# Optimization experiments

Hardware: AMD Instinct MI355X
Metric: run time of the kernel (lower is better)

The kernel has to match this reference:

```python
import jax, jax.numpy as jnp
import numpy as np

B, N, D, S, H, ITERS = 128, 4096, 64, 7, 128, 3
EPS = 1e-8
LN_EPS = 1e-5


def _ln(x, g, b):
    mu = jnp.mean(x, axis=-1, keepdims=True)
    var = jnp.mean(jnp.square(x - mu), axis=-1, keepdims=True)
    return (x - mu) * jax.lax.rsqrt(var + LN_EPS) * g + b


def setup_inputs() -> dict:
    key = jax.random.key(0)
    ks = jax.random.split(key, 20)
    xav = lambda k, shp: jax.random.normal(k, shp, jnp.float32) * (2.0 / sum(shp[-2:])) ** 0.5
    inp = {
        "inputs": jax.random.normal(ks[0], (B, N, D), jnp.float32),
        "noise_bg": jax.random.normal(ks[1], (B, 1, D), jnp.float32),
        "noise_fg": jax.random.normal(ks[2], (B, S - 1, D), jnp.float32),
        "ln_in_g": jnp.ones((D,), jnp.float32), "ln_in_b": jnp.zeros((D,), jnp.float32),
        "ln_slot_g": jnp.ones((D,), jnp.float32), "ln_slot_b": jnp.zeros((D,), jnp.float32),
        "ln_mlp_g": jnp.ones((D,), jnp.float32), "ln_mlp_b": jnp.zeros((D,), jnp.float32),
        "Wq": xav(ks[3], (D, D)), "Wk": xav(ks[4], (D, D)), "Wv": xav(ks[5], (D, D)),
        "W_ih": xav(ks[6], (3 * D, D)), "W_hh": xav(ks[7], (3 * D, D)),
        "b_ih": jnp.zeros((3 * D,), jnp.float32), "b_hh": jnp.zeros((3 * D,), jnp.float32),
        "mlp_w1": xav(ks[8], (H, D)), "mlp_b1": jnp.zeros((H,), jnp.float32),
        "mlp_w2": xav(ks[9], (D, H)), "mlp_b2": jnp.zeros((D,), jnp.float32),
        "slots_bg_mu": xav(ks[10], (1, 1, D)),
        "slots_bg_log_sigma": xav(ks[11], (1, 1, D)),
        "slots_mu": xav(ks[12], (1, 1, D)),
        "slots_log_sigma": xav(ks[13], (1, 1, D)),
    }
    return inp


def _gru(x, h, W_ih, W_hh, b_ih, b_hh):
    # x, h: [M, D]; PyTorch GRUCell math, gate order r, z, n
    gi = x @ W_ih.T + b_ih
    gh = h @ W_hh.T + b_hh
    i_r, i_z, i_n = jnp.split(gi, 3, axis=-1)
    h_r, h_z, h_n = jnp.split(gh, 3, axis=-1)
    r = jax.nn.sigmoid(i_r + h_r)
    z = jax.nn.sigmoid(i_z + h_z)
    n = jnp.tanh(i_n + r * h_n)
    return (1.0 - z) * n + z * h


def reference(inputs, noise_bg, noise_fg, ln_in_g, ln_in_b, ln_slot_g, ln_slot_b,
              ln_mlp_g, ln_mlp_b, Wq, Wk, Wv, W_ih, W_hh, b_ih, b_hh,
              mlp_w1, mlp_b1, mlp_w2, mlp_b2,
              slots_bg_mu, slots_bg_log_sigma, slots_mu, slots_log_sigma):
    x = _ln(inputs, ln_in_g, ln_in_b)          # [B, N, D]
    k = jnp.einsum('bnd,ed->bne', x, Wk)       # [B, N, D]
    v = jnp.einsum('bnd,ed->bne', x, Wv)

    bg = slots_bg_mu + jnp.exp(slots_bg_log_sigma) * noise_bg   # [B, 1, D]
    fg = slots_mu + jnp.exp(slots_log_sigma) * noise_fg          # [B, S-1, D]
    slots = jnp.concatenate([bg, fg], axis=1)                    # [B, S, D]

    scale = D ** (-0.5)
    for _ in range(ITERS):
        slots_prev = slots
        s = _ln(slots, ln_slot_g, ln_slot_b)
        q = jnp.einsum('bsd,ed->bse', s, Wq)                     # [B, S, D]
        logits = scale * jnp.einsum('bnd,bsd->bns', k, q)        # [B, N, S]
        attn = jax.nn.softmax(logits, axis=-1) + EPS             # softmax over slots
        attn = attn / jnp.sum(attn, axis=1, keepdims=True)       # renorm over inputs
        updates = jnp.einsum('bns,bnd->bsd', attn, v)            # [B, S, D]
        h = _gru(updates.reshape(B * S, D), slots_prev.reshape(B * S, D),
                 W_ih, W_hh, b_ih, b_hh).reshape(B, S, D)
        m = _ln(h, ln_mlp_g, ln_mlp_b)
        m = jax.nn.relu(m @ mlp_w1.T + mlp_b1) @ mlp_w2.T + mlp_b2
        slots = h + m
    return slots
```

## Files before the change

kernel.cpp:

```cpp
#include <hip/hip_runtime.h>

#define BB 128
#define NN 4096
#define DD 64
#define SS 7
#define HH 128
#define N_ITERS 3
#define EPS_ATTN 1e-8f
#define LN_EPS 1e-5f

typedef unsigned short ushortT;
using short8  = __attribute__((ext_vector_type(8))) short;
using floatx4 = __attribute__((ext_vector_type(4))) float;

__device__ __forceinline__ float bf2f(int u) {
    return __builtin_bit_cast(float, (unsigned)(u & 0xffff) << 16);
}
__device__ __forceinline__ ushortT f2bf(float f) {
    unsigned x = __builtin_bit_cast(unsigned, f);
    x = x + 0x7fff + ((x >> 16) & 1);
    return (ushortT)(x >> 16);
}
__device__ __forceinline__ void wave_stats64(float x, float& mu, float& var) {
    float s1 = x, s2 = x * x;
#pragma unroll
    for (int off = 32; off > 0; off >>= 1) {
        s1 += __shfl_xor(s1, off);
        s2 += __shfl_xor(s2, off);
    }
    mu  = s1 * (1.f / 64.f);
    var = s2 * (1.f / 64.f) - mu * mu;
}

__global__ void prep_w(const float* __restrict__ Wk, const float* __restrict__ Wv,
                       const float* __restrict__ Wih, const float* __restrict__ Whh,
                       const float* __restrict__ w1, const float* __restrict__ w2,
                       ushortT* __restrict__ Wkvf, float* __restrict__ WihT,
                       float* __restrict__ WhhT, float* __restrict__ w1T,
                       float* __restrict__ w2T) {
    int i = blockIdx.x * 256 + threadIdx.x;
    if (i < 8192) {
        int c2 = i >> 9, lane = (i >> 3) & 63, j = i & 7;
        int tile = c2 >> 1, cc = c2 & 1;
        int qd = lane >> 4, m = lane & 15;
        int row = tile * 16 + m;
        int col = cc * 32 + qd * 8 + j;
        float v = (row < 64) ? Wk[row * 64 + col] : Wv[(row - 64) * 64 + col];
        Wkvf[i] = f2bf(v);
    } else if (i < 20480) {
        int j = i - 8192; int e = j >> 6, d = j & 63;
        WihT[d * 192 + e] = Wih[j];
    } else if (i < 32768) {
        int j = i - 20480; int e = j >> 6, d = j & 63;
        WhhT[d * 192 + e] = Whh[j];
    } else if (i < 40960) {
        int j = i - 32768; int e = j >> 6, d = j & 63;
        w1T[d * 128 + e] = w1[j];
    } else if (i < 49152) {
        int j = i - 40960; int e = j >> 7, h = j & 127;
        w2T[h * 64 + e] = w2[j];
    }
}

__global__ __launch_bounds__(256) void kv_proj(const float* __restrict__ x,
                                               const float* __restrict__ g,
                                               const float* __restrict__ bta,
                                               const ushortT* __restrict__ Wkvf,
                                               ushortT* __restrict__ kg,
                                               ushortT* __restrict__ vtg) {
    int t = threadIdx.x, w = t >> 6, lane = t & 63;
    long row0 = (long)blockIdx.x << 6;
    int sub = t & 3, r = t >> 2;
    __shared__ ushortT lds_a[64][72];

    const float* xr = x + (row0 + r) * 64 + sub * 16;
    float4 xa[4];
#pragma unroll
    for (int c = 0; c < 4; ++c) xa[c] = *reinterpret_cast<const float4*>(xr + c * 4);
    float s1 = 0.f, s2 = 0.f;
#pragma unroll
    for (int c = 0; c < 4; ++c) {
        s1 += xa[c].x + xa[c].y + xa[c].z + xa[c].w;
        s2 += xa[c].x * xa[c].x + xa[c].y * xa[c].y +
              xa[c].z * xa[c].z + xa[c].w * xa[c].w;
    }
    s1 += __shfl_xor(s1, 1); s2 += __shfl_xor(s2, 1);
    s1 += __shfl_xor(s1, 2); s2 += __shfl_xor(s2, 2);
    float mu = s1 * (1.f / 64.f);
    float var = s2 * (1.f / 64.f) - mu * mu;
    float rs = rsqrtf(var + LN_EPS);
    unsigned un[8];
#pragma unroll
    for (int c = 0; c < 4; ++c) {
        float4 g4 = *reinterpret_cast<const float4*>(g + sub * 16 + c * 4);
        float4 b4 = *reinterpret_cast<const float4*>(bta + sub * 16 + c * 4);
        float n0 = (xa[c].x - mu) * rs * g4.x + b4.x;
        float n1 = (xa[c].y - mu) * rs * g4.y + b4.y;
        float n2 = (xa[c].z - mu) * rs * g4.z + b4.z;
        float n3 = (xa[c].w - mu) * rs * g4.w + b4.w;
        un[c * 2]     = (unsigned)f2bf(n0) | ((unsigned)f2bf(n1) << 16);
        un[c * 2 + 1] = (unsigned)f2bf(n2) | ((unsigned)f2bf(n3) << 16);
    }
    *reinterpret_cast<uint4*>(&lds_a[r][sub * 16]) =
        make_uint4(un[0], un[1], un[2], un[3]);
    *reinterpret_cast<uint4*>(&lds_a[r][sub * 16 + 8]) =
        make_uint4(un[4], un[5], un[6], un[7]);

    int m = lane & 15, qd = lane >> 4;
    short8 bk[4][2];
#pragma unroll
    for (int tt = 0; tt < 4; ++tt)
#pragma unroll
        for (int c = 0; c < 2; ++c)
            bk[tt][c] = *reinterpret_cast<const short8*>(
                Wkvf + (tt * 2 + c) * 512 + lane * 8);
    __syncthreads();

    short8 af[2];
#pragma unroll
    for (int c = 0; c < 2; ++c)
        af[c] = *reinterpret_cast<const short8*>(&lds_a[w * 16 + m][c * 32 + qd * 8]);

    floatx4 ak[4];
#pragma unroll
    for (int tt = 0; tt < 4; ++tt) ak[tt] = (floatx4){0.f, 0.f, 0.f, 0.f};
#pragma unroll
    for (int tt = 0; tt < 4; ++tt)
#pragma unroll
        for (int c = 0; c < 2; ++c)
            ak[tt] = __builtin_amdgcn_mfma_f32_16x16x32_bf16(bk[tt][c], af[c],
                                                             ak[tt], 0, 0, 0);
    long kbase = ((long)blockIdx.x << 12) + w * 1024 + lane * 4;
#pragma unroll
    for (int tt = 0; tt < 4; ++tt) {
        uint2 u;
        u.x = (unsigned)f2bf(ak[tt][0]) | ((unsigned)f2bf(ak[tt][1]) << 16);
        u.y = (unsigned)f2bf(ak[tt][2]) | ((unsigned)f2bf(ak[tt][3]) << 16);
        *reinterpret_cast<uint2*>(kg + kbase + tt * 256) = u;
    }

    short8 bv[4][2];
#pragma unroll
    for (int tt = 0; tt < 4; ++tt)
#pragma unroll
        for (int c = 0; c < 2; ++c)
            bv[tt][c] = *reinterpret_cast<const short8*>(
                Wkvf + ((tt + 4) * 2 + c) * 512 + lane * 8);
    floatx4 av[4];
#pragma unroll
    for (int tt = 0; tt < 4; ++tt) av[tt] = (floatx4){0.f, 0.f, 0.f, 0.f};
#pragma unroll
    for (int tt = 0; tt < 4; ++tt)
#pragma unroll
        for (int c = 0; c < 2; ++c)
            av[tt] = __builtin_amdgcn_mfma_f32_16x16x32_bf16(af[c], bv[tt][c],
                                                             av[tt], 0, 0, 0);
    int ks  = (((int)(row0 & 127)) + w * 16) >> 5;
    int qd2 = (w * 2 + (qd >> 1)) & 3;
    long vbase = (((long)blockIdx.x >> 1) << 13) + ks * 512 + qd2 * 128 + m * 8 +
                 (qd & 1) * 4;
#pragma unroll
    for (int tt = 0; tt < 4; ++tt) {
        uint2 u;
        u.x = (unsigned)f2bf(av[tt][0]) | ((unsigned)f2bf(av[tt][1]) << 16);
        u.y = (unsigned)f2bf(av[tt][2]) | ((unsigned)f2bf(av[tt][3]) << 16);
        *reinterpret_cast<uint2*>(vtg + vbase + tt * 2048) = u;
    }
}

__global__ __launch_bounds__(256) void attn_kernel(const ushortT* __restrict__ kg,
                                                   const ushortT* __restrict__ vtg,
                                                   const float* __restrict__ qbuf,
                                                   float* __restrict__ num_p,
                                                   float* __restrict__ den_p) {
    int t = threadIdx.x;
    int ck = blockIdx.x;
    int b = ck >> 5;
    __shared__ float   q_lds[7][68];
    __shared__ ushortT p_lds[16][136];
    __shared__ float   den_w[4][8];
    int w = t >> 6, lane = t & 63, m = lane & 15, qd = lane >> 4;
    int sub = t & 3, rr = t >> 2;

    uint2 kf[2][4];
#pragma unroll
    for (int p = 0; p < 2; ++p) {
        const ushortT* kp = kg + ((long)(ck * 2 + p) << 12) + w * 1024 +
                            sub * 256 + (lane >> 2) * 4;
#pragma unroll
        for (int dq = 0; dq < 4; ++dq)
            kf[p][dq] = *reinterpret_cast<const uint2*>(kp + dq * 64);
    }
    const ushortT* vb = vtg + ((long)ck << 13) + w * 2048 + lane * 8;
    short8 bf[4];
#pragma unroll
    for (int ks = 0; ks < 4; ++ks)
        bf[ks] = *reinterpret_cast<const short8*>(vb + ks * 512);
    for (int i = t; i < 448; i += 256) q_lds[i >> 6][i & 63] = qbuf[b * 448 + i];
    __syncthreads();

    float dreg0 = 0.f, dreg1 = 0.f;
    int s0 = sub * 2;
#pragma unroll
    for (int p = 0; p < 2; ++p) {
        int row = p * 64 + rr;
        float kx[16];
#pragma unroll
        for (int dq = 0; dq < 4; ++dq) {
            kx[dq * 4 + 0] = bf2f(kf[p][dq].x);
            kx[dq * 4 + 1] = bf2f(kf[p][dq].x >> 16);
            kx[dq * 4 + 2] = bf2f(kf[p][dq].y);
            kx[dq * 4 + 3] = bf2f(kf[p][dq].y >> 16);
        }
        float lg[7];
#pragma unroll
        for (int s = 0; s < 7; ++s) {
            const float4* qp = reinterpret_cast<const float4*>(&q_lds[s][sub << 4]);
            float acc = 0.f;
#pragma unroll
            for (int c = 0; c < 4; ++c) {
                float4 qv = qp[c];
                acc += kx[c * 4 + 0] * qv.x + kx[c * 4 + 1] * qv.y +
                       kx[c * 4 + 2] * qv.z + kx[c * 4 + 3] * qv.w;
            }
            lg[s] = acc;
        }
#pragma unroll
        for (int s = 0; s < 7; ++s) {
            lg[s] += __shfl_xor(lg[s], 1);
            lg[s] += __shfl_xor(lg[s], 2);
        }
        float mx = lg[0];
#pragma unroll
        for (int s = 1; s < 7; ++s) mx = fmaxf(mx, lg[s]);
        float sum = 0.f, ps[7];
#pragma unroll
        for (int s = 0; s < 7; ++s) { ps[s] = __expf(lg[s] - mx); sum += ps[s]; }
        float inv = 1.f / sum;
        float p0 = 0.f, p1 = 0.f;
#pragma unroll
        for (int s = 0; s < 7; ++s) {
            float pv = ps[s] * inv + EPS_ATTN;
            if (s == s0)     p0 = pv;
            if (s == s0 + 1) p1 = pv;
        }
        ushortT pb0 = f2bf(p0);
        p_lds[s0][row] = pb0;
        dreg0 += bf2f(pb0);
        if (sub < 3) {
            ushortT pb1 = f2bf(p1);
            p_lds[s0 + 1][row] = pb1;
            dreg1 += bf2f(pb1);
        }
    }
#pragma unroll
    for (int off = 4; off < 64; off <<= 1) {
        dreg0 += __shfl_xor(dreg0, off);
        dreg1 += __shfl_xor(dreg1, off);
    }
    if (lane < 4) {
        den_w[w][2 * lane] = dreg0;
        if (lane < 3) den_w[w][2 * lane + 1] = dreg1;
    }
    __syncthreads();

    floatx4 acc = (floatx4){0.f, 0.f, 0.f, 0.f};
#pragma unroll
    for (int ks = 0; ks < 4; ++ks) {
        short8 af = *reinterpret_cast<const short8*>(&p_lds[m][ks * 32 + qd * 8]);
        acc = __builtin_amdgcn_mfma_f32_16x16x32_bf16(af, bf[ks], acc, 0, 0, 0);
    }
#pragma unroll
    for (int r = 0; r < 4; ++r) {
        int s = qd * 4 + r;
        if (s < 7) num_p[((long)ck * 7 + s) * 64 + w * 16 + m] = acc[r];
    }
    if (t < 7) den_p[ck * 8 + t] = den_w[0][t] + den_w[1][t] + den_w[2][t] + den_w[3][t];
}

__global__ __launch_bounds__(448) void slot_update_q(
    int mode,
    const float* __restrict__ num_p, const float* __restrict__ den_p,
    float* __restrict__ slots,
    const float* __restrict__ nbg, const float* __restrict__ nfg,
    const float* __restrict__ bgmu, const float* __restrict__ bgls,
    const float* __restrict__ fmu, const float* __restrict__ fls,
    const float* __restrict__ WihT, const float* __restrict__ WhhT,
    const float* __restrict__ bih, const float* __restrict__ bhh,
    const float* __restrict__ lng, const float* __restrict__ lnb,
    const float* __restrict__ w1T, const float* __restrict__ b1,
    const float* __restrict__ w2T, const float* __restrict__ b2,
    const float* __restrict__ Wq,
    const float* __restrict__ sg, const float* __restrict__ sb,
    float* __restrict__ qbuf, float* __restrict__ outp) {
    int b = blockIdx.x, t = threadIdx.x, s = t >> 6, l = t & 63;
    __shared__ float WqT[64 * 65];
    __shared__ float updL[7][64], hprevL[7][64], mnL[7][64], m1L[7][128], xnL[7][64];
    if (mode != 2)
        for (int i = t; i < 4096; i += 448)
            WqT[(i & 63) * 65 + (i >> 6)] = Wq[i];
    float res;
    if (mode == 0) {
        float v;
        if (s == 0) v = bgmu[l] + __expf(bgls[l]) * nbg[b * 64 + l];
        else        v = fmu[l]  + __expf(fls[l])  * nfg[(b * 6 + s - 1) * 64 + l];
        res = v;
        __syncthreads();
    } else {
        float nsum = 0.f, dsum = 0.f;
#pragma unroll 4
        for (int c = 0; c < 32; ++c) {
            nsum += num_p[((long)(b * 32 + c) * 7 + s) * 64 + l];
            dsum += den_p[(b * 32 + c) * 8 + s];
        }
        float hp = slots[(b * 7 + s) * 64 + l];
        updL[s][l]   = nsum / dsum;
        hprevL[s][l] = hp;
        __syncthreads();
        float gi0 = bih[l], gi1 = bih[64 + l], gi2 = bih[128 + l];
        float gh0 = bhh[l], gh1 = bhh[64 + l], gh2 = bhh[128 + l];
#pragma unroll 8
        for (int d = 0; d < 64; ++d) {
            float u = updL[s][d], hh = hprevL[s][d];
            gi0 += u * WihT[d * 192 + l];
            gi1 += u * WihT[d * 192 + 64 + l];
            gi2 += u * WihT[d * 192 + 128 + l];
            gh0 += hh * WhhT[d * 192 + l];
            gh1 += hh * WhhT[d * 192 + 64 + l];
            gh2 += hh * WhhT[d * 192 + 128 + l];
        }
        float r = 1.f / (1.f + __expf(-(gi0 + gh0)));
        float z = 1.f / (1.f + __expf(-(gi1 + gh1)));
        float n = tanhf(gi2 + r * gh2);
        float h = (1.f - z) * n + z * hp;
        float mu, var;
        wave_stats64(h, mu, var);
        mnL[s][l] = (h - mu) * rsqrtf(var + LN_EPS) * lng[l] + lnb[l];
        float a0 = b1[l], a1 = b1[64 + l];
#pragma unroll 8
        for (int d = 0; d < 64; ++d) {
            float mv = mnL[s][d];
            a0 += mv * w1T[d * 128 + l];
            a1 += mv * w1T[d * 128 + 64 + l];
        }
        m1L[s][l]      = fmaxf(a0, 0.f);
        m1L[s][64 + l] = fmaxf(a1, 0.f);
        float a2 = b2[l];
#pragma unroll 8
        for (int h2 = 0; h2 < 128; ++h2) a2 += m1L[s][h2] * w2T[h2 * 64 + l];
        res = h + a2;
    }
    slots[(b * 7 + s) * 64 + l] = res;
    if (mode == 2) {
        outp[(b * 7 + s) * 64 + l] = res;
        return;
    }
    float mu, var;
    wave_stats64(res, mu, var);
    xnL[s][l] = (res - mu) * rsqrtf(var + LN_EPS) * sg[l] + sb[l];
    float acc = 0.f;
#pragma unroll 8
    for (int d = 0; d < 64; ++d) acc += xnL[s][d] * WqT[d * 65 + l];
    qbuf[(b * 7 + s) * 64 + l] = acc * 0.125f;
}

extern "C" void kernel_launch(void* const* d_in, const int* in_sizes, int n_in,
                              void* d_out, int out_size, void* d_ws, size_t ws_size,
                              hipStream_t stream) {
    const float* inputs    = (const float*)d_in[0];
    const float* noise_bg  = (const float*)d_in[1];
    const float* noise_fg  = (const float*)d_in[2];
    const float* ln_in_g   = (const float*)d_in[3];
    const float* ln_in_b   = (const float*)d_in[4];
    const float* ln_slot_g = (const float*)d_in[5];
    const float* ln_slot_b = (const float*)d_in[6];
    const float* ln_mlp_g  = (const float*)d_in[7];
    const float* ln_mlp_b  = (const float*)d_in[8];
    const float* Wq        = (const float*)d_in[9];
    const float* Wk        = (const float*)d_in[10];
    const float* Wv        = (const float*)d_in[11];
    const float* W_ih      = (const float*)d_in[12];
    const float* W_hh      = (const float*)d_in[13];
    const float* b_ih      = (const float*)d_in[14];
    const float* b_hh      = (const float*)d_in[15];
    const float* mlp_w1    = (const float*)d_in[16];
    const float* mlp_b1    = (const float*)d_in[17];
    const float* mlp_w2    = (const float*)d_in[18];
    const float* mlp_b2    = (const float*)d_in[19];
    const float* sbg_mu    = (const float*)d_in[20];
    const float* sbg_ls    = (const float*)d_in[21];
    const float* s_mu      = (const float*)d_in[22];
    const float* s_ls      = (const float*)d_in[23];

    char* ws = (char*)d_ws;
    size_t off = 0;
    auto alloc = [&](size_t bytes) {
        void* p = ws + off;
        off += (bytes + 255) & ~(size_t)255;
        return p;
    };
    ushortT* kg    = (ushortT*)alloc((size_t)BB * NN * 64 * 2);
    ushortT* vtg   = (ushortT*)alloc((size_t)BB * NN * 64 * 2);
    ushortT* Wkvf  = (ushortT*)alloc(8192 * 2);
    float* slots   = (float*)alloc(57344 * 4);
    float* qbuf    = (float*)alloc(57344 * 4);
    float* num_p   = (float*)alloc((size_t)4096 * 7 * 64 * 4);
    float* den_p   = (float*)alloc(4096 * 8 * 4);
    float* WihT    = (float*)alloc(12288 * 4);
    float* WhhT    = (float*)alloc(12288 * 4);
    float* w1T     = (float*)alloc(8192 * 4);
    float* w2T     = (float*)alloc(8192 * 4);
    if (off > ws_size) return;

    prep_w<<<192, 256, 0, stream>>>(Wk, Wv, W_ih, W_hh, mlp_w1, mlp_w2,
                                    Wkvf, WihT, WhhT, w1T, w2T);
    slot_update_q<<<128, 448, 0, stream>>>(0, num_p, den_p, slots,
                                           noise_bg, noise_fg, sbg_mu, sbg_ls,
                                           s_mu, s_ls, WihT, WhhT, b_ih, b_hh,
                                           ln_mlp_g, ln_mlp_b, w1T, mlp_b1,
                                           w2T, mlp_b2, Wq, ln_slot_g, ln_slot_b,
                                           qbuf, (float*)d_out);
    kv_proj<<<8192, 256, 0, stream>>>(inputs, ln_in_g, ln_in_b, Wkvf, kg, vtg);
    for (int it = 0; it < N_ITERS; ++it) {
        attn_kernel<<<4096, 256, 0, stream>>>(kg, vtg, qbuf, num_p, den_p);
        slot_update_q<<<128, 448, 0, stream>>>((it == N_ITERS - 1) ? 2 : 1,
                                               num_p, den_p, slots,
                                               noise_bg, noise_fg, sbg_mu, sbg_ls,
                                               s_mu, s_ls, WihT, WhhT, b_ih, b_hh,
                                               ln_mlp_g, ln_mlp_b, w1T, mlp_b1,
                                               w2T, mlp_b2, Wq, ln_slot_g, ln_slot_b,
                                               qbuf, (float*)d_out);
    }
}
```

Baseline: 399.4 us.

## Fold Wk and Wv projections into slot-side math, attend directly on normalized inputs

Removes the separate K/V projection kernel. The logits are computed as xn·(Wkᵀq), with q pre-multiplied by Wk in the slot kernel, and the attention-weighted sum is taken over xn and then multiplied by Wv once per slot. The first attention pass fuses the input layernorm and stores a bf16 normalized copy of the inputs, which later passes reuse. This replaces two bf16 K/V tensors with one, so each iteration reads half the data. The cost is an LDS transpose of xn inside each attention block and small extra matvecs in the slot update.

```diff
diff --git a/kernel.cpp b/kernel.cpp
--- a/kernel.cpp
+++ b/kernel.cpp
@@ -13,8 +13,8 @@
 using short8  = __attribute__((ext_vector_type(8))) short;
 using floatx4 = __attribute__((ext_vector_type(4))) float;
 
-__device__ __forceinline__ float bf2f(int u) {
-    return __builtin_bit_cast(float, (unsigned)(u & 0xffff) << 16);
+__device__ __forceinline__ float bf2f(unsigned u) {
+    return __builtin_bit_cast(float, (u & 0xffffu) << 16);
 }
 __device__ __forceinline__ ushortT f2bf(float f) {
     unsigned x = __builtin_bit_cast(unsigned, f);
@@ -32,190 +32,123 @@
     var = s2 * (1.f / 64.f) - mu * mu;
 }
 
-__global__ void prep_w(const float* __restrict__ Wk, const float* __restrict__ Wv,
-                       const float* __restrict__ Wih, const float* __restrict__ Whh,
+__global__ void prep_w(const float* __restrict__ Wih, const float* __restrict__ Whh,
                        const float* __restrict__ w1, const float* __restrict__ w2,
-                       ushortT* __restrict__ Wkvf, float* __restrict__ WihT,
-                       float* __restrict__ WhhT, float* __restrict__ w1T,
-                       float* __restrict__ w2T) {
+                       const float* __restrict__ Wv,
+                       float* __restrict__ WihT, float* __restrict__ WhhT,
+                       float* __restrict__ w1T, float* __restrict__ w2T,
+                       float* __restrict__ WvT) {
     int i = blockIdx.x * 256 + threadIdx.x;
-    if (i < 8192) {
-        int c2 = i >> 9, lane = (i >> 3) & 63, j = i & 7;
-        int tile = c2 >> 1, cc = c2 & 1;
-        int qd = lane >> 4, m = lane & 15;
-        int row = tile * 16 + m;
-        int col = cc * 32 + qd * 8 + j;
-        float v = (row < 64) ? Wk[row * 64 + col] : Wv[(row - 64) * 64 + col];
-        Wkvf[i] = f2bf(v);
-    } else if (i < 20480) {
-        int j = i - 8192; int e = j >> 6, d = j & 63;
-        WihT[d * 192 + e] = Wih[j];
+    if (i < 12288) {
+        int e = i >> 6, d = i & 63;
+        WihT[d * 192 + e] = Wih[i];
+    } else if (i < 24576) {
+        int j = i - 12288; int e = j >> 6, d = j & 63;
+        WhhT[d * 192 + e] = Whh[j];
     } else if (i < 32768) {
-        int j = i - 20480; int e = j >> 6, d = j & 63;
-        WhhT[d * 192 + e] = Whh[j];
+        int j = i - 24576; int e = j >> 6, d = j & 63;
+        w1T[d * 128 + e] = w1[j];
     } else if (i < 40960) {
-        int j = i - 32768; int e = j >> 6, d = j & 63;
-        w1T[d * 128 + e] = w1[j];
-    } else if (i < 49152) {
-        int j = i - 40960; int e = j >> 7, h = j & 127;
+        int j = i - 32768; int e = j >> 7, h = j & 127;
         w2T[h * 64 + e] = w2[j];
-    }
-}
-
-__global__ __launch_bounds__(256) void kv_proj(const float* __restrict__ x,
-                                               const float* __restrict__ g,
-                                               const float* __restrict__ bta,
-                                               const ushortT* __restrict__ Wkvf,
-                                               ushortT* __restrict__ kg,
-                                               ushortT* __restrict__ vtg) {
-    int t = threadIdx.x, w = t >> 6, lane = t & 63;
-    long row0 = (long)blockIdx.x << 6;
-    int sub = t & 3, r = t >> 2;
-    __shared__ ushortT lds_a[64][72];
-
-    const float* xr = x + (row0 + r) * 64 + sub * 16;
-    float4 xa[4];
-#pragma unroll
-    for (int c = 0; c < 4; ++c) xa[c] = *reinterpret_cast<const float4*>(xr + c * 4);
-    float s1 = 0.f, s2 = 0.f;
-#pragma unroll
-    for (int c = 0; c < 4; ++c) {
-        s1 += xa[c].x + xa[c].y + xa[c].z + xa[c].w;
-        s2 += xa[c].x * xa[c].x + xa[c].y * xa[c].y +
-              xa[c].z * xa[c].z + xa[c].w * xa[c].w;
-    }
-    s1 += __shfl_xor(s1, 1); s2 += __shfl_xor(s2, 1);
-    s1 += __shfl_xor(s1, 2); s2 += __shfl_xor(s2, 2);
-    float mu = s1 * (1.f / 64.f);
-    float var = s2 * (1.f / 64.f) - mu * mu;
-    float rs = rsqrtf(var + LN_EPS);
-    unsigned un[8];
-#pragma unroll
-    for (int c = 0; c < 4; ++c) {
-        float4 g4 = *reinterpret_cast<const float4*>(g + sub * 16 + c * 4);
-        float4 b4 = *reinterpret_cast<const float4*>(bta + sub * 16 + c * 4);
-        float n0 = (xa[c].x - mu) * rs * g4.x + b4.x;
-        float n1 = (xa[c].y - mu) * rs * g4.y + b4.y;
-        float n2 = (xa[c].z - mu) * rs * g4.z + b4.z;
-        float n3 = (xa[c].w - mu) * rs * g4.w + b4.w;
-        un[c * 2]     = (unsigned)f2bf(n0) | ((unsigned)f2bf(n1) << 16);
-        un[c * 2 + 1] = (unsigned)f2bf(n2) | ((unsigned)f2bf(n3) << 16);
-    }
-    *reinterpret_cast<uint4*>(&lds_a[r][sub * 16]) =
-        make_uint4(un[0], un[1], un[2], un[3]);
-    *reinterpret_cast<uint4*>(&lds_a[r][sub * 16 + 8]) =
-        make_uint4(un[4], un[5], un[6], un[7]);
-
-    int m = lane & 15, qd = lane >> 4;
-    short8 bk[4][2];
-#pragma unroll
-    for (int tt = 0; tt < 4; ++tt)
-#pragma unroll
-        for (int c = 0; c < 2; ++c)
-            bk[tt][c] = *reinterpret_cast<const short8*>(
-                Wkvf + (tt * 2 + c) * 512 + lane * 8);
-    __syncthreads();
-
-    short8 af[2];
-#pragma unroll
-    for (int c = 0; c < 2; ++c)
-        af[c] = *reinterpret_cast<const short8*>(&lds_a[w * 16 + m][c * 32 + qd * 8]);
-
-    floatx4 ak[4];
-#pragma unroll
-    for (int tt = 0; tt < 4; ++tt) ak[tt] = (floatx4){0.f, 0.f, 0.f, 0.f};
-#pragma unroll
-    for (int tt = 0; tt < 4; ++tt)
-#pragma unroll
-        for (int c = 0; c < 2; ++c)
-            ak[tt] = __builtin_amdgcn_mfma_f32_16x16x32_bf16(bk[tt][c], af[c],
-                                                             ak[tt], 0, 0, 0);
-    long kbase = ((long)blockIdx.x << 12) + w * 1024 + lane * 4;
-#pragma unroll
-    for (int tt = 0; tt < 4; ++tt) {
-        uint2 u;
-        u.x = (unsigned)f2bf(ak[tt][0]) | ((unsigned)f2bf(ak[tt][1]) << 16);
-        u.y = (unsigned)f2bf(ak[tt][2]) | ((unsigned)f2bf(ak[tt][3]) << 16);
-        *reinterpret_cast<uint2*>(kg + kbase + tt * 256) = u;
-    }
-
-    short8 bv[4][2];
-#pragma unroll
-    for (int tt = 0; tt < 4; ++tt)
-#pragma unroll
-        for (int c = 0; c < 2; ++c)
-            bv[tt][c] = *reinterpret_cast<const short8*>(
-                Wkvf + ((tt + 4) * 2 + c) * 512 + lane * 8);
-    floatx4 av[4];
-#pragma unroll
-    for (int tt = 0; tt < 4; ++tt) av[tt] = (floatx4){0.f, 0.f, 0.f, 0.f};
-#pragma unroll
-    for (int tt = 0; tt < 4; ++tt)
-#pragma unroll
-        for (int c = 0; c < 2; ++c)
-            av[tt] = __builtin_amdgcn_mfma_f32_16x16x32_bf16(af[c], bv[tt][c],
-                                                             av[tt], 0, 0, 0);
-    int ks  = (((int)(row0 & 127)) + w * 16) >> 5;
-    int qd2 = (w * 2 + (qd >> 1)) & 3;
-    long vbase = (((long)blockIdx.x >> 1) << 13) + ks * 512 + qd2 * 128 + m * 8 +
-                 (qd & 1) * 4;
-#pragma unroll
-    for (int tt = 0; tt < 4; ++tt) {
-        uint2 u;
-        u.x = (unsigned)f2bf(av[tt][0]) | ((unsigned)f2bf(av[tt][1]) << 16);
-        u.y = (unsigned)f2bf(av[tt][2]) | ((unsigned)f2bf(av[tt][3]) << 16);
-        *reinterpret_cast<uint2*>(vtg + vbase + tt * 2048) = u;
-    }
-}
-
-__global__ __launch_bounds__(256) void attn_kernel(const ushortT* __restrict__ kg,
-                                                   const ushortT* __restrict__ vtg,
-                                                   const float* __restrict__ qbuf,
-                                                   float* __restrict__ num_p,
-                                                   float* __restrict__ den_p) {
+    } else if (i < 45056) {
+        int j = i - 40960; int d = j >> 6, e = j & 63;
+        WvT[e * 64 + d] = Wv[j];
+    }
+}
+
+__global__ __launch_bounds__(256) void attn_kernel(
+    int first,
+    const float* __restrict__ x,
+    const float* __restrict__ lng, const float* __restrict__ lnb,
+    ushortT* __restrict__ xnf,
+    const float* __restrict__ qkbuf,
+    float* __restrict__ pxn_p, float* __restrict__ den_p) {
     int t = threadIdx.x;
-    int ck = blockIdx.x;
-    int b = ck >> 5;
-    __shared__ float   q_lds[7][68];
+    int ck = blockIdx.x, b = ck >> 5;
+    int w = t >> 6, lane = t & 63, m = lane & 15, qd = lane >> 4;
+    int sub = t & 3, rr = t >> 2;
+    __shared__ float   qk_lds[7][68];
+    __shared__ ushortT xnT[64][136];
     __shared__ ushortT p_lds[16][136];
     __shared__ float   den_w[4][8];
-    int w = t >> 6, lane = t & 63, m = lane & 15, qd = lane >> 4;
-    int sub = t & 3, rr = t >> 2;
-
-    uint2 kf[2][4];
-#pragma unroll
-    for (int p = 0; p < 2; ++p) {
-        const ushortT* kp = kg + ((long)(ck * 2 + p) << 12) + w * 1024 +
-                            sub * 256 + (lane >> 2) * 4;
-#pragma unroll
-        for (int dq = 0; dq < 4; ++dq)
-            kf[p][dq] = *reinterpret_cast<const uint2*>(kp + dq * 64);
-    }
-    const ushortT* vb = vtg + ((long)ck << 13) + w * 2048 + lane * 8;
-    short8 bf[4];
-#pragma unroll
-    for (int ks = 0; ks < 4; ++ks)
-        bf[ks] = *reinterpret_cast<const short8*>(vb + ks * 512);
-    for (int i = t; i < 448; i += 256) q_lds[i >> 6][i & 63] = qbuf[b * 448 + i];
+
+    unsigned xw[2][8];
+    if (first) {
+        float4 g4[4], b4[4];
+#pragma unroll
+        for (int c = 0; c < 4; ++c) {
+            g4[c] = *reinterpret_cast<const float4*>(lng + sub * 16 + c * 4);
+            b4[c] = *reinterpret_cast<const float4*>(lnb + sub * 16 + c * 4);
+        }
+#pragma unroll
+        for (int pass = 0; pass < 2; ++pass) {
+            const float* xr = x + ((long)ck * 128 + pass * 64 + rr) * 64 + sub * 16;
+            float4 xa[4];
+#pragma unroll
+            for (int c = 0; c < 4; ++c)
+                xa[c] = *reinterpret_cast<const float4*>(xr + c * 4);
+            float s1 = 0.f, s2 = 0.f;
+#pragma unroll
+            for (int c = 0; c < 4; ++c) {
+                s1 += xa[c].x + xa[c].y + xa[c].z + xa[c].w;
+                s2 += xa[c].x * xa[c].x + xa[c].y * xa[c].y +
+                      xa[c].z * xa[c].z + xa[c].w * xa[c].w;
+            }
+            s1 += __shfl_xor(s1, 1); s2 += __shfl_xor(s2, 1);
+            s1 += __shfl_xor(s1, 2); s2 += __shfl_xor(s2, 2);
+            float mu = s1 * (1.f / 64.f);
+            float var = s2 * (1.f / 64.f) - mu * mu;
+            float rs = rsqrtf(var + LN_EPS);
+#pragma unroll
+            for (int c = 0; c < 4; ++c) {
+                float n0 = (xa[c].x - mu) * rs * g4[c].x + b4[c].x;
+                float n1 = (xa[c].y - mu) * rs * g4[c].y + b4[c].y;
+                float n2 = (xa[c].z - mu) * rs * g4[c].z + b4[c].z;
+                float n3 = (xa[c].w - mu) * rs * g4[c].w + b4[c].w;
+                xw[pass][c * 2]     = (unsigned)f2bf(n0) | ((unsigned)f2bf(n1) << 16);
+                xw[pass][c * 2 + 1] = (unsigned)f2bf(n2) | ((unsigned)f2bf(n3) << 16);
+            }
+            ushortT* xp = xnf + (long)ck * 8192 + pass * 4096 + t * 16;
+            *reinterpret_cast<uint4*>(xp) =
+                make_uint4(xw[pass][0], xw[pass][1], xw[pass][2], xw[pass][3]);
+            *reinterpret_cast<uint4*>(xp + 8) =
+                make_uint4(xw[pass][4], xw[pass][5], xw[pass][6], xw[pass][7]);
+        }
+    } else {
+#pragma unroll
+        for (int pass = 0; pass < 2; ++pass) {
+            const ushortT* xp = xnf + (long)ck * 8192 + pass * 4096 + t * 16;
+            uint4 u0 = *reinterpret_cast<const uint4*>(xp);
+            uint4 u1 = *reinterpret_cast<const uint4*>(xp + 8);
+            xw[pass][0] = u0.x; xw[pass][1] = u0.y;
+            xw[pass][2] = u0.z; xw[pass][3] = u0.w;
+            xw[pass][4] = u1.x; xw[pass][5] = u1.y;
+            xw[pass][6] = u1.z; xw[pass][7] = u1.w;
+        }
+    }
+    for (int i = t; i < 448; i += 256) qk_lds[i >> 6][i & 63] = qkbuf[b * 448 + i];
     __syncthreads();
 
     float dreg0 = 0.f, dreg1 = 0.f;
     int s0 = sub * 2;
 #pragma unroll
-    for (int p = 0; p < 2; ++p) {
-        int row = p * 64 + rr;
+    for (int pass = 0; pass < 2; ++pass) {
+        int row = pass * 64 + rr;
+#pragma unroll
+        for (int j = 0; j < 16; ++j)
+            xnT[sub * 16 + j][row] =
+                (ushortT)(xw[pass][j >> 1] >> ((j & 1) * 16));
         float kx[16];
 #pragma unroll
-        for (int dq = 0; dq < 4; ++dq) {
-            kx[dq * 4 + 0] = bf2f(kf[p][dq].x);
-            kx[dq * 4 + 1] = bf2f(kf[p][dq].x >> 16);
-            kx[dq * 4 + 2] = bf2f(kf[p][dq].y);
-            kx[dq * 4 + 3] = bf2f(kf[p][dq].y >> 16);
+        for (int j = 0; j < 8; ++j) {
+            kx[2 * j]     = bf2f(xw[pass][j]);
+            kx[2 * j + 1] = bf2f(xw[pass][j] >> 16);
         }
         float lg[7];
 #pragma unroll
         for (int s = 0; s < 7; ++s) {
-            const float4* qp = reinterpret_cast<const float4*>(&q_lds[s][sub << 4]);
+            const float4* qp = reinterpret_cast<const float4*>(&qk_lds[s][sub << 4]);
             float acc = 0.f;
 #pragma unroll
             for (int c = 0; c < 4; ++c) {
@@ -268,19 +201,20 @@
 #pragma unroll
     for (int ks = 0; ks < 4; ++ks) {
         short8 af = *reinterpret_cast<const short8*>(&p_lds[m][ks * 32 + qd * 8]);
-        acc = __builtin_amdgcn_mfma_f32_16x16x32_bf16(af, bf[ks], acc, 0, 0, 0);
+        short8 bf = *reinterpret_cast<const short8*>(&xnT[w * 16 + m][ks * 32 + qd * 8]);
+        acc = __builtin_amdgcn_mfma_f32_16x16x32_bf16(af, bf, acc, 0, 0, 0);
     }
 #pragma unroll
     for (int r = 0; r < 4; ++r) {
         int s = qd * 4 + r;
-        if (s < 7) num_p[((long)ck * 7 + s) * 64 + w * 16 + m] = acc[r];
+        if (s < 7) pxn_p[((long)ck * 7 + s) * 64 + w * 16 + m] = acc[r];
     }
     if (t < 7) den_p[ck * 8 + t] = den_w[0][t] + den_w[1][t] + den_w[2][t] + den_w[3][t];
 }
 
 __global__ __launch_bounds__(448) void slot_update_q(
     int mode,
-    const float* __restrict__ num_p, const float* __restrict__ den_p,
+    const float* __restrict__ pxn_p, const float* __restrict__ den_p,
     float* __restrict__ slots,
     const float* __restrict__ nbg, const float* __restrict__ nfg,
     const float* __restrict__ bgmu, const float* __restrict__ bgls,
@@ -290,12 +224,14 @@
     const float* __restrict__ lng, const float* __restrict__ lnb,
     const float* __restrict__ w1T, const float* __restrict__ b1,
     const float* __restrict__ w2T, const float* __restrict__ b2,
+    const float* __restrict__ WvT, const float* __restrict__ Wk,
     const float* __restrict__ Wq,
     const float* __restrict__ sg, const float* __restrict__ sb,
-    float* __restrict__ qbuf, float* __restrict__ outp) {
+    float* __restrict__ qkbuf, float* __restrict__ outp) {
     int b = blockIdx.x, t = threadIdx.x, s = t >> 6, l = t & 63;
     __shared__ float WqT[64 * 65];
-    __shared__ float updL[7][64], hprevL[7][64], mnL[7][64], m1L[7][128], xnL[7][64];
+    __shared__ float pxnL[7][64], updL[7][64], hprevL[7][64], mnL[7][64],
+                     xnL[7][64], qL[7][64], m1L[7][128];
     if (mode != 2)
         for (int i = t; i < 4096; i += 448)
             WqT[(i & 63) * 65 + (i >> 6)] = Wq[i];
@@ -307,15 +243,19 @@
         res = v;
         __syncthreads();
     } else {
-        float nsum = 0.f, dsum = 0.f;
+        float psum = 0.f, dsum = 0.f;
 #pragma unroll 4
         for (int c = 0; c < 32; ++c) {
-            nsum += num_p[((long)(b * 32 + c) * 7 + s) * 64 + l];
+            psum += pxn_p[((long)(b * 32 + c) * 7 + s) * 64 + l];
             dsum += den_p[(b * 32 + c) * 8 + s];
         }
+        pxnL[s][l] = psum;
         float hp = slots[(b * 7 + s) * 64 + l];
-        updL[s][l]   = nsum / dsum;
         hprevL[s][l] = hp;
+        float nm = 0.f;
+#pragma unroll 8
+        for (int e = 0; e < 64; ++e) nm += pxnL[s][e] * WvT[e * 64 + l];
+        updL[s][l] = nm / dsum;
         __syncthreads();
         float gi0 = bih[l], gi1 = bih[64 + l], gi2 = bih[128 + l];
         float gh0 = bhh[l], gh1 = bhh[64 + l], gh2 = bhh[128 + l];
@@ -358,10 +298,14 @@
     float mu, var;
     wave_stats64(res, mu, var);
     xnL[s][l] = (res - mu) * rsqrtf(var + LN_EPS) * sg[l] + sb[l];
-    float acc = 0.f;
-#pragma unroll 8
-    for (int d = 0; d < 64; ++d) acc += xnL[s][d] * WqT[d * 65 + l];
-    qbuf[(b * 7 + s) * 64 + l] = acc * 0.125f;
+    float qv = 0.f;
+#pragma unroll 8
+    for (int d = 0; d < 64; ++d) qv += xnL[s][d] * WqT[d * 65 + l];
+    qL[s][l] = qv * 0.125f;
+    float qk = 0.f;
+#pragma unroll 8
+    for (int e = 0; e < 64; ++e) qk += qL[s][e] * Wk[e * 64 + l];
+    qkbuf[(b * 7 + s) * 64 + l] = qk;
 }
 
 extern "C" void kernel_launch(void* const* d_in, const int* in_sizes, int n_in,
@@ -399,36 +343,38 @@
         off += (bytes + 255) & ~(size_t)255;
         return p;
     };
-    ushortT* kg    = (ushortT*)alloc((size_t)BB * NN * 64 * 2);
-    ushortT* vtg   = (ushortT*)alloc((size_t)BB * NN * 64 * 2);
-    ushortT* Wkvf  = (ushortT*)alloc(8192 * 2);
+    ushortT* xnf   = (ushortT*)alloc((size_t)BB * NN * 64 * 2);
     float* slots   = (float*)alloc(57344 * 4);
-    float* qbuf    = (float*)alloc(57344 * 4);
-    float* num_p   = (float*)alloc((size_t)4096 * 7 * 64 * 4);
+    float* qkbuf   = (float*)alloc(57344 * 4);
+    float* pxn_p   = (float*)alloc((size_t)4096 * 7 * 64 * 4);
     float* den_p   = (float*)alloc(4096 * 8 * 4);
     float* WihT    = (float*)alloc(12288 * 4);
     float* WhhT    = (float*)alloc(12288 * 4);
     float* w1T     = (float*)alloc(8192 * 4);
     float* w2T     = (float*)alloc(8192 * 4);
+    float* WvT     = (float*)alloc(4096 * 4);
     if (off > ws_size) return;
 
-    prep_w<<<192, 256, 0, stream>>>(Wk, Wv, W_ih, W_hh, mlp_w1, mlp_w2,
-                                    Wkvf, WihT, WhhT, w1T, w2T);
-    slot_update_q<<<128, 448, 0, stream>>>(0, num_p, den_p, slots,
+    prep_w<<<176, 256, 0, stream>>>(W_ih, W_hh, mlp_w1, mlp_w2, Wv,
+                                    WihT, WhhT, w1T, w2T, WvT);
+    slot_update_q<<<128, 448, 0, stream>>>(0, pxn_p, den_p, slots,
                                            noise_bg, noise_fg, sbg_mu, sbg_ls,
                                            s_mu, s_ls, WihT, WhhT, b_ih, b_hh,
                                            ln_mlp_g, ln_mlp_b, w1T, mlp_b1,
-                                           w2T, mlp_b2, Wq, ln_slot_g, ln_slot_b,
-                                           qbuf, (float*)d_out);
-    kv_proj<<<8192, 256, 0, stream>>>(inputs, ln_in_g, ln_in_b, Wkvf, kg, vtg);
+                                           w2T, mlp_b2, WvT, Wk, Wq,
+                                           ln_slot_g, ln_slot_b,
+                                           qkbuf, (float*)d_out);
     for (int it = 0; it < N_ITERS; ++it) {
-        attn_kernel<<<4096, 256, 0, stream>>>(kg, vtg, qbuf, num_p, den_p);
+        attn_kernel<<<4096, 256, 0, stream>>>((it == 0) ? 1 : 0,
+                                              inputs, ln_in_g, ln_in_b,
+                                              xnf, qkbuf, pxn_p, den_p);
         slot_update_q<<<128, 448, 0, stream>>>((it == N_ITERS - 1) ? 2 : 1,
-                                               num_p, den_p, slots,
+                                               pxn_p, den_p, slots,
                                                noise_bg, noise_fg, sbg_mu, sbg_ls,
                                                s_mu, s_ls, WihT, WhhT, b_ih, b_hh,
                                                ln_mlp_g, ln_mlp_b, w1T, mlp_b1,
-                                               w2T, mlp_b2, Wq, ln_slot_g, ln_slot_b,
-                                               qbuf, (float*)d_out);
-    }
-}
+                                               w2T, mlp_b2, WvT, Wk, Wq,
+                                               ln_slot_g, ln_slot_b,
+                                               qkbuf, (float*)d_out);
+    }
+}
```

New measurement: 382.6 us. 4.2% less time.
